# Kernel optimization log

Measured on AMD Instinct MI355X. Metric: run time of the kernel, lower is better.

Reference implementation:

```python
import jax, jax.numpy as jnp
import numpy as np

KERNEL = 11  # matches AttnBlock(kernel_size=11)
EPS = 1e-4


def _patches(x, k):
    """Extract k x k patches (stride 1, VALID), matching nn.Unfold ordering.

    x: [B, C, H, W] -> ([B, L, C*k*k], (Hp, Wp)) with L = Hp*Wp.
    """
    p = jax.lax.conv_general_dilated_patches(x, (k, k), (1, 1), 'VALID')  # [B, C*k*k, Hp, Wp]
    B, D, Hp, Wp = p.shape
    return p.reshape(B, D, Hp * Wp).transpose(0, 2, 1), (Hp, Wp)


def setup_inputs() -> dict:
    key = jax.random.key(0)
    k1, k2 = jax.random.split(key)
    im1 = jax.random.normal(k1, (4, 64, 40, 40), dtype=jnp.float32)
    im2 = jax.random.normal(k2, (4, 64, 40, 40), dtype=jnp.float32)
    return {"im1": im1, "im2": im2}


def reference(im1, im2):
    k = KERNEL
    # Dynamic per-sample filters from im1 patches, L2-normalized per patch.
    p1, _ = _patches(im1, k)                                  # [B, L, D], D = C*k*k
    norm = jnp.sqrt(jnp.sum(p1 * p1, axis=-1, keepdims=True))  # [B, L, 1]
    p1n = p1 / jnp.maximum(norm, EPS)
    # conv2d(im2, filters) with stride 1 / no padding == dot of im2 patches with filters.
    p2, (Hp, Wp) = _patches(im2, k)                           # [B, P, D], P = Hp*Wp
    scores = jnp.einsum('bld,bpd->bpl', p1n, p2)              # [B, P, L]
    out = jnp.max(scores, axis=-1)                            # max over filter (channel) dim
    B = im1.shape[0]
    return out.reshape(B, 1, Hp, Wp)
```

## Files before the change

kernel.cpp:

```cpp
#include <hip/hip_runtime.h>

#define C_    64
#define H_    40
#define W_    40
#define KS    11
#define HP    30
#define NB    4
#define NL    900
#define ND    59
#define EPSF  1e-4f
#define PCH   6
#define SCW   65
#define NINF  -3.4e38f
#define MPAD  1664
#define GSTEP 66600

typedef _Float16 f16x8 __attribute__((ext_vector_type(8)));
typedef float    f32x4 __attribute__((ext_vector_type(4)));

__global__ __launch_bounds__(1024)
void k_pack(const float* __restrict__ im2, const float* __restrict__ im1,
            _Float16* __restrict__ packed, float* __restrict__ invnorm) {
    const int b = blockIdx.x, img = blockIdx.y;
    const int tid = threadIdx.x;
    __shared__ float ssq[1600];
    __shared__ float colsum[1200];
    const float* src = (img ? im1 : im2) + b * C_ * 1600;
    _Float16* dst = packed + ((size_t)img * NB + b) * (8 * MPAD * 8);
    for (int pos = tid; pos < MPAD; pos += 1024) {
        float ss = 0.f;
        #pragma unroll
        for (int oct = 0; oct < 8; ++oct) {
            f16x8 h = {};
            if (pos < 1600) {
                #pragma unroll
                for (int j = 0; j < 8; ++j) {
                    float v = src[(oct * 8 + j) * 1600 + pos];
                    h[j] = (_Float16)v;
                    ss += v * v;
                }
            }
            *(f16x8*)&dst[(oct * MPAD + pos) * 8] = h;
        }
        if (img == 1 && pos < 1600) ssq[pos] = ss;
    }
    if (img != 1) return;
    __syncthreads();
    for (int t = tid; t < HP * W_; t += 1024) {
        int yy = t / W_, x = t - yy * W_;
        float s = 0.f;
        #pragma unroll
        for (int r = 0; r < KS; ++r) s += ssq[(yy + r) * W_ + x];
        colsum[t] = s;
    }
    __syncthreads();
    for (int t = tid; t < NL; t += 1024) {
        int ly = t / HP, lx = t - ly * HP;
        float s = 0.f;
        #pragma unroll
        for (int sx = 0; sx < KS; ++sx) s += colsum[ly * W_ + lx + sx];
        invnorm[b * NL + t] = 1.f / fmaxf(sqrtf(s), EPSF);
    }
}

__global__ __launch_bounds__(256, 3)
void k_gram(const _Float16* __restrict__ packed, _Float16* __restrict__ G) {
    const int i = blockIdx.x, j = blockIdx.y, b = blockIdx.z;
    int dd = i - j; if (dd < 0) dd = -dd;
    if (dd > 10) return;
    const int tid = threadIdx.x;
    const int w = tid >> 6, L = tid & 63, lq = L >> 4, lr = L & 15;

    __shared__ __align__(16) _Float16 smem[128 * 136];
    _Float16 (*As)[128][8] = (_Float16 (*)[128][8])smem;
    _Float16 (*Bs)[128][8] = (_Float16 (*)[128][8])(smem + 8192);

    const _Float16* pa = packed + (size_t)b * (8 * MPAD * 8);
    const _Float16* pb = packed + (size_t)(NB + b) * (8 * MPAD * 8);
    for (int t = tid; t < 1024; t += 256) {
        int oct = t >> 7, m = t & 127;
        *(f16x8*)&As[oct][m][0] = *(const f16x8*)&pa[(oct * MPAD + i * 128 + m) * 8];
        *(f16x8*)&Bs[oct][m][0] = *(const f16x8*)&pb[(oct * MPAD + j * 128 + m) * 8];
    }
    __syncthreads();

    const int mb = (w & 1) * 64, nb = (w >> 1) * 64;
    f16x8 a0[4], a1[4], b0[4], b1[4];
    #pragma unroll
    for (int q = 0; q < 4; ++q) {
        a0[q] = *(const f16x8*)&As[lq][mb + q * 16 + lr][0];
        a1[q] = *(const f16x8*)&As[4 + lq][mb + q * 16 + lr][0];
        b0[q] = *(const f16x8*)&Bs[lq][nb + q * 16 + lr][0];
        b1[q] = *(const f16x8*)&Bs[4 + lq][nb + q * 16 + lr][0];
    }
    f32x4 acc[4][4];
    #pragma unroll
    for (int mi = 0; mi < 4; ++mi)
        #pragma unroll
        for (int ni = 0; ni < 4; ++ni) {
            f32x4 c = {0.f, 0.f, 0.f, 0.f};
            c = __builtin_amdgcn_mfma_f32_16x16x32_f16(a0[mi], b0[ni], c, 0, 0, 0);
            c = __builtin_amdgcn_mfma_f32_16x16x32_f16(a1[mi], b1[ni], c, 0, 0, 0);
            acc[mi][ni] = c;
        }
    __syncthreads();
    #pragma unroll
    for (int mi = 0; mi < 4; ++mi)
        #pragma unroll
        for (int ni = 0; ni < 4; ++ni)
            #pragma unroll
            for (int rg = 0; rg < 4; ++rg)
                smem[(mb + mi * 16 + lq * 4 + rg) * 136 + nb + ni * 16 + lr] =
                    (_Float16)acc[mi][ni][rg];
    __syncthreads();
    _Float16* Gb = G + (size_t)b * (MPAD * MPAD);
    for (int t = tid; t < 2048; t += 256) {
        int row = t >> 4, seg = t & 15;
        *(f16x8*)&Gb[(size_t)(i * 128 + row) * MPAD + j * 128 + seg * 8] =
            *(const f16x8*)&smem[row * 136 + seg * 8];
    }
}

__global__ __launch_bounds__(256, 4)
void k_box(const _Float16* __restrict__ G, const float* __restrict__ invnorm,
           unsigned int* __restrict__ keys) {
    const int chunk = blockIdx.x;
    const int dy = (int)blockIdx.y - (HP - 1);
    const int b = blockIdx.z;
    const int ady = dy < 0 ? -dy : dy;
    const int rows = HP - ady;
    if (chunk * PCH >= rows) return;
    const int pyLo = dy < 0 ? -dy : 0;
    const int py0 = pyLo + chunk * PCH;
    const int P = min(PCH, rows - chunk * PCH);
    const int tid = threadIdx.x;

    __shared__ float csum[1600];
    __shared__ float scratch[HP * SCW];
    __shared__ float partials[120];
    __shared__ float sInv[HP];

    const _Float16* Gb = G + (size_t)b * (MPAD * MPAD);
    float s[8];
    const _Float16* base = nullptr;
    if (tid < 200) {
        int e = tid * 8, x2 = e / 40, x1 = e - x2 * 40;
        base = Gb + (size_t)py0 * GSTEP + x2 * MPAD + dy * 40 + x1;
        #pragma unroll
        for (int j = 0; j < 8; ++j) s[j] = 0.f;
        for (int r = 0; r < KS; ++r) {
            f16x8 q = *(const f16x8*)(base + r * GSTEP);
            #pragma unroll
            for (int j = 0; j < 8; ++j) s[j] += (float)q[j];
        }
    }

    for (int i = 0; i < P; ++i) {
        const int py = py0 + i, ly = py + dy;
        if (tid < 200) {
            if (i > 0) {
                f16x8 qa = *(const f16x8*)(base + (i + 10) * GSTEP);
                f16x8 qs = *(const f16x8*)(base + (i - 1) * GSTEP);
                #pragma unroll
                for (int j = 0; j < 8; ++j) s[j] += (float)qa[j] - (float)qs[j];
            }
            float4* c4 = (float4*)(csum + tid * 8);
            c4[0] = make_float4(s[0], s[1], s[2], s[3]);
            c4[1] = make_float4(s[4], s[5], s[6], s[7]);
        } else if (tid >= 224 && tid < 224 + HP) {
            sInv[tid - 224] = invnorm[b * NL + ly * HP + (tid - 224)];
        }
        __syncthreads();
        for (int t = tid; t < 5 * ND; t += 256) {
            int pg = t / ND, dxI = t - ND * pg;
            int dx = dxI - (HP - 1), pxb = 6 * pg;
            #pragma unroll
            for (int u = 0; u < 6; ++u) scratch[(pxb + u) * SCW + dxI] = NINF;
            int u0 = max(0, -dx - pxb), u1 = min(5, (HP - 1) - dx - pxb);
            if (u0 <= u1) {
                const float* cp = csum + dx;
                float run = 0.f;
                #pragma unroll
                for (int sr = 0; sr < KS; ++sr) run += cp[(pxb + u0 + sr) * (W_ + 1)];
                int u = u0;
                for (;;) {
                    scratch[(pxb + u) * SCW + dxI] = run * sInv[pxb + u + dx];
                    if (++u > u1) break;
                    run += cp[(pxb + u + 10) * (W_ + 1)] - cp[(pxb + u - 1) * (W_ + 1)];
                }
            }
        }
        __syncthreads();
        if (tid < 120) {
            int px = tid >> 2, q = tid & 3;
            float m = NINF;
            int d0 = q * 15, d1 = min(d0 + 15, ND);
            for (int d = d0; d < d1; ++d) m = fmaxf(m, scratch[px * SCW + d]);
            partials[tid] = m;
        }
        __syncthreads();
        if (tid < HP) {
            float m = fmaxf(fmaxf(partials[tid * 4], partials[tid * 4 + 1]),
                            fmaxf(partials[tid * 4 + 2], partials[tid * 4 + 3]));
            unsigned int ub = __float_as_uint(m);
            unsigned int k = (ub & 0x80000000u) ? ~ub : (ub | 0x80000000u);
            atomicMax(&keys[b * NL + py * HP + tid], k);
        }
        __syncthreads();
    }
}

__global__ __launch_bounds__(256)
void k_decode(const unsigned int* __restrict__ keys, float* __restrict__ out) {
    int i = blockIdx.x * 256 + threadIdx.x;
    if (i < NB * NL) {
        unsigned int k = keys[i];
        unsigned int u = (k & 0x80000000u) ? (k ^ 0x80000000u) : ~k;
        out[i] = __uint_as_float(u);
    }
}

__global__ __launch_bounds__(256)
void k_norm_fb(const float* __restrict__ im1, float* __restrict__ invnorm) {
    const int ly = blockIdx.x, b = blockIdx.y;
    const int tid = threadIdx.x;
    __shared__ float colsq[KS * W_];
    __shared__ float colsum[W_];
    const float* base = im1 + b * C_ * H_ * W_;
    for (int i = tid; i < KS * W_; i += 256) {
        int r = i / W_, x = i - r * W_;
        const float* p = base + (ly + r) * W_ + x;
        float s = 0.f;
        #pragma unroll 8
        for (int c = 0; c < C_; ++c) { float v = p[c * H_ * W_]; s += v * v; }
        colsq[i] = s;
    }
    __syncthreads();
    if (tid < W_) {
        float s = 0.f;
        #pragma unroll
        for (int r = 0; r < KS; ++r) s += colsq[r * W_ + tid];
        colsum[tid] = s;
    }
    __syncthreads();
    if (tid < HP) {
        float s = 0.f;
        #pragma unroll
        for (int sx = 0; sx < KS; ++sx) s += colsum[tid + sx];
        invnorm[b * NL + ly * HP + tid] = 1.f / fmaxf(sqrtf(s), EPSF);
    }
}

#define MAXPL 16
__global__ __launch_bounds__(256, 2)
void k_main_fb(const float* __restrict__ im1, const float* __restrict__ im2,
               const float* __restrict__ invnorm, unsigned int* __restrict__ keys) {
    const int chunk = blockIdx.x;
    const int dy = (int)blockIdx.y - (HP - 1);
    const int b = blockIdx.z;
    const int ady = dy < 0 ? -dy : dy;
    const int rows = HP - ady;
    if (chunk * PCH >= rows) return;
    const int pyLo = dy < 0 ? -dy : 0;
    const int py0 = pyLo + chunk * PCH;
    const int P = min(PCH, rows - chunk * PCH);
    const int nPl = P + KS - 1;
    const int tid = threadIdx.x;
    const int w = tid >> 6, L = tid & 63, lq = L >> 4, lr = L & 15;

    __shared__ __align__(16) _Float16 planes[MAXPL][H_ * W_];
    __shared__ __align__(16) float csum[H_ * W_];
    __shared__ __align__(16) _Float16 Astg[8][48][8];
    __shared__ __align__(16) _Float16 Bstg[8][48][8];
    __shared__ float scratch[HP * SCW];
    __shared__ float partials[120];
    __shared__ float sInv[HP];

    const float* im1b = im1 + b * C_ * H_ * W_;
    const float* im2b = im2 + b * C_ * H_ * W_;
    if (tid < 128) {
        int arr = tid >> 6, r = tid & 63;
        int oct = r >> 3, x = 40 + (r & 7);
        f16x8 z = {};
        *(f16x8*)((arr ? Bstg : Astg)[oct][x]) = z;
    }
    for (int p = 0; p < nPl; ++p) {
        const int y = py0 + p;
        for (int t = tid; t < 640; t += 256) {
            int arr = t >= 320;
            int r = arr ? t - 320 : t;
            int oct = r / 40, x = r - oct * 40;
            const float* pc = (arr ? (im1b + (y + dy) * W_) : (im2b + y * W_))
                              + oct * 8 * H_ * W_ + x;
            f16x8 h;
            #pragma unroll
            for (int j = 0; j < 8; ++j) h[j] = (_Float16)pc[j * H_ * W_];
            *(f16x8*)((arr ? Bstg : Astg)[oct][x]) = h;
        }
        __syncthreads();
        for (int t = w; t < 9; t += 4) {
            int mt = t / 3, nt = t - 3 * mt;
            f16x8 a0 = *(const f16x8*)(Astg[lq][mt * 16 + lr]);
            f16x8 b0 = *(const f16x8*)(Bstg[lq][nt * 16 + lr]);
            f16x8 a1 = *(const f16x8*)(Astg[4 + lq][mt * 16 + lr]);
            f16x8 b1 = *(const f16x8*)(Bstg[4 + lq][nt * 16 + lr]);
            f32x4 acc = {0.f, 0.f, 0.f, 0.f};
            acc = __builtin_amdgcn_mfma_f32_16x16x32_f16(a0, b0, acc, 0, 0, 0);
            acc = __builtin_amdgcn_mfma_f32_16x16x32_f16(a1, b1, acc, 0, 0, 0);
            int x1 = nt * 16 + lr;
            if (x1 < W_) {
                int x2b = mt * 16 + lq * 4;
                #pragma unroll
                for (int rg = 0; rg < 4; ++rg) {
                    int x2 = x2b + rg;
                    if (x2 < W_) planes[p][x2 * W_ + x1] = (_Float16)acc[rg];
                }
            }
        }
        __syncthreads();
    }
    for (int i = 0; i < P; ++i) {
        const int py = py0 + i, ly = py + dy;
        if (tid < 200) {
            float4* c4 = (float4*)(csum + tid * 8);
            if (i == 0) {
                float s[8] = {0.f,0.f,0.f,0.f,0.f,0.f,0.f,0.f};
                #pragma unroll
                for (int r = 0; r < KS; ++r) {
                    f16x8 q = *(const f16x8*)(planes[r] + tid * 8);
                    #pragma unroll
                    for (int j = 0; j < 8; ++j) s[j] += (float)q[j];
                }
                c4[0] = make_float4(s[0], s[1], s[2], s[3]);
                c4[1] = make_float4(s[4], s[5], s[6], s[7]);
            } else {
                f16x8 qa = *(const f16x8*)(planes[i + 10] + tid * 8);
                f16x8 qs = *(const f16x8*)(planes[i - 1] + tid * 8);
                float4 v0 = c4[0], v1 = c4[1];
                v0.x += (float)qa[0] - (float)qs[0]; v0.y += (float)qa[1] - (float)qs[1];
                v0.z += (float)qa[2] - (float)qs[2]; v0.w += (float)qa[3] - (float)qs[3];
                v1.x += (float)qa[4] - (float)qs[4]; v1.y += (float)qa[5] - (float)qs[5];
                v1.z += (float)qa[6] - (float)qs[6]; v1.w += (float)qa[7] - (float)qs[7];
                c4[0] = v0; c4[1] = v1;
            }
        } else if (tid >= 224 && tid < 224 + HP) {
            sInv[tid - 224] = invnorm[b * NL + ly * HP + (tid - 224)];
        }
        __syncthreads();
        for (int t = tid; t < 5 * ND; t += 256) {
            int pg = t / ND, dxI = t - ND * pg;
            int dx = dxI - (HP - 1), pxb = 6 * pg;
            #pragma unroll
            for (int u = 0; u < 6; ++u) scratch[(pxb + u) * SCW + dxI] = NINF;
            int u0 = max(0, -dx - pxb), u1 = min(5, (HP - 1) - dx - pxb);
            if (u0 <= u1) {
                const float* cp = csum + dx;
                float run = 0.f;
                #pragma unroll
                for (int sr = 0; sr < KS; ++sr) run += cp[(pxb + u0 + sr) * (W_ + 1)];
                int u = u0;
                for (;;) {
                    scratch[(pxb + u) * SCW + dxI] = run * sInv[pxb + u + dx];
                    if (++u > u1) break;
                    run += cp[(pxb + u + 10) * (W_ + 1)] - cp[(pxb + u - 1) * (W_ + 1)];
                }
            }
        }
        __syncthreads();
        if (tid < 120) {
            int px = tid >> 2, q = tid & 3;
            float m = NINF;
            int d0 = q * 15, d1 = min(d0 + 15, ND);
            for (int d = d0; d < d1; ++d) m = fmaxf(m, scratch[px * SCW + d]);
            partials[tid] = m;
        }
        __syncthreads();
        if (tid < HP) {
            float m = fmaxf(fmaxf(partials[tid * 4], partials[tid * 4 + 1]),
                            fmaxf(partials[tid * 4 + 2], partials[tid * 4 + 3]));
            unsigned int ub = __float_as_uint(m);
            unsigned int k = (ub & 0x80000000u) ? ~ub : (ub | 0x80000000u);
            atomicMax(&keys[b * NL + py * HP + tid], k);
        }
        __syncthreads();
    }
}

extern "C" void kernel_launch(void* const* d_in, const int* in_sizes, int n_in,
                              void* d_out, int out_size, void* d_ws, size_t ws_size,
                              hipStream_t stream) {
    const float* im1 = (const float*)d_in[0];
    const float* im2 = (const float*)d_in[1];
    unsigned int* keys = (unsigned int*)d_ws;
    float* invnorm = (float*)d_ws + NB * NL;
    const size_t packedOff = 32768;
    const size_t packedBytes = (size_t)2 * NB * 8 * MPAD * 8 * 2;
    const size_t gOff = packedOff + packedBytes;
    const size_t gBytes = (size_t)NB * MPAD * MPAD * 2;
    const size_t needed = gOff + gBytes;

    hipMemsetAsync(d_ws, 0, NB * NL * sizeof(unsigned int), stream);
    if (ws_size >= needed) {
        _Float16* packed = (_Float16*)((char*)d_ws + packedOff);
        _Float16* G = (_Float16*)((char*)d_ws + gOff);
        k_pack<<<dim3(NB, 2), 1024, 0, stream>>>(im2, im1, packed, invnorm);
        k_gram<<<dim3(13, 13, NB), 256, 0, stream>>>(packed, G);
        k_box<<<dim3(5, ND, NB), 256, 0, stream>>>(G, invnorm, keys);
    } else {
        k_norm_fb<<<dim3(HP, NB), 256, 0, stream>>>(im1, invnorm);
        k_main_fb<<<dim3(5, ND, NB), 256, 0, stream>>>(im1, im2, invnorm, keys);
    }
    k_decode<<<(NB * NL + 255) / 256, 256, 0, stream>>>(keys, (float*)d_out);
}
```

Measured before the change: 110.3 us.

## Spread packing over many blocks, fold key clearing in, prefetch box loads

The pack kernel used to run as 8 blocks of 1024 threads. It is now split across 104 small blocks and writes per-position sums of squares to a buffer. A separate small k_norm kernel turns those sums into inverse patch norms. Key zeroing moves into the pack kernel, so the memset is dropped from the fast path. In k_box, the inverse norms for every row are loaded once up front, the next row's sliding-window G loads are issued before the barrier so they overlap the scan, and the trailing barrier in each row loop is removed. The cost is one extra kernel launch in exchange for better GPU occupancy during packing and less latency in the box stage.

```diff
diff --git a/kernel.cpp b/kernel.cpp
--- a/kernel.cpp
+++ b/kernel.cpp
@@ -18,33 +18,38 @@
 typedef _Float16 f16x8 __attribute__((ext_vector_type(8)));
 typedef float    f32x4 __attribute__((ext_vector_type(4)));
 
+__global__ __launch_bounds__(128)
+void k_pack(const float* __restrict__ im2, const float* __restrict__ im1,
+            _Float16* __restrict__ packed, float* __restrict__ ssqbuf,
+            unsigned int* __restrict__ keys) {
+    const int blk = blockIdx.x, b = blockIdx.y, img = blockIdx.z;
+    const int pos = blk * 128 + threadIdx.x;
+    const float* src = (img ? im1 : im2) + b * C_ * 1600;
+    _Float16* dst = packed + ((size_t)img * NB + b) * (8 * MPAD * 8);
+    float ss = 0.f;
+    #pragma unroll
+    for (int oct = 0; oct < 8; ++oct) {
+        f16x8 h = {};
+        if (pos < 1600) {
+            #pragma unroll
+            for (int j = 0; j < 8; ++j) {
+                float v = src[(oct * 8 + j) * 1600 + pos];
+                h[j] = (_Float16)v;
+                ss += v * v;
+            }
+        }
+        *(f16x8*)&dst[(oct * MPAD + pos) * 8] = h;
+    }
+    if (img == 1 && pos < 1600) ssqbuf[b * 1600 + pos] = ss;
+    if (img == 0 && pos < NL) keys[b * NL + pos] = 0u;
+}
+
 __global__ __launch_bounds__(1024)
-void k_pack(const float* __restrict__ im2, const float* __restrict__ im1,
-            _Float16* __restrict__ packed, float* __restrict__ invnorm) {
-    const int b = blockIdx.x, img = blockIdx.y;
-    const int tid = threadIdx.x;
+void k_norm(const float* __restrict__ ssqbuf, float* __restrict__ invnorm) {
+    const int b = blockIdx.x, tid = threadIdx.x;
     __shared__ float ssq[1600];
     __shared__ float colsum[1200];
-    const float* src = (img ? im1 : im2) + b * C_ * 1600;
-    _Float16* dst = packed + ((size_t)img * NB + b) * (8 * MPAD * 8);
-    for (int pos = tid; pos < MPAD; pos += 1024) {
-        float ss = 0.f;
-        #pragma unroll
-        for (int oct = 0; oct < 8; ++oct) {
-            f16x8 h = {};
-            if (pos < 1600) {
-                #pragma unroll
-                for (int j = 0; j < 8; ++j) {
-                    float v = src[(oct * 8 + j) * 1600 + pos];
-                    h[j] = (_Float16)v;
-                    ss += v * v;
-                }
-            }
-            *(f16x8*)&dst[(oct * MPAD + pos) * 8] = h;
-        }
-        if (img == 1 && pos < 1600) ssq[pos] = ss;
-    }
-    if (img != 1) return;
+    for (int i = tid; i < 1600; i += 1024) ssq[i] = ssqbuf[b * 1600 + i];
     __syncthreads();
     for (int t = tid; t < HP * W_; t += 1024) {
         int yy = t / W_, x = t - yy * W_;
@@ -138,10 +143,16 @@
     __shared__ float csum[1600];
     __shared__ float scratch[HP * SCW];
     __shared__ float partials[120];
-    __shared__ float sInv[HP];
+    __shared__ float sInvAll[PCH][HP];
+
+    if (tid < P * HP) {
+        int i = tid / HP, lx = tid - i * HP;
+        sInvAll[i][lx] = invnorm[b * NL + (py0 + i + dy) * HP + lx];
+    }
 
     const _Float16* Gb = G + (size_t)b * (MPAD * MPAD);
     float s[8];
+    f16x8 qa, qs;
     const _Float16* base = nullptr;
     if (tid < 200) {
         int e = tid * 8, x2 = e / 40, x1 = e - x2 * 40;
@@ -156,19 +167,19 @@
     }
 
     for (int i = 0; i < P; ++i) {
-        const int py = py0 + i, ly = py + dy;
+        const int py = py0 + i;
         if (tid < 200) {
             if (i > 0) {
-                f16x8 qa = *(const f16x8*)(base + (i + 10) * GSTEP);
-                f16x8 qs = *(const f16x8*)(base + (i - 1) * GSTEP);
                 #pragma unroll
                 for (int j = 0; j < 8; ++j) s[j] += (float)qa[j] - (float)qs[j];
             }
             float4* c4 = (float4*)(csum + tid * 8);
             c4[0] = make_float4(s[0], s[1], s[2], s[3]);
             c4[1] = make_float4(s[4], s[5], s[6], s[7]);
-        } else if (tid >= 224 && tid < 224 + HP) {
-            sInv[tid - 224] = invnorm[b * NL + ly * HP + (tid - 224)];
+            if (i + 1 < P) {
+                qa = *(const f16x8*)(base + (i + 11) * GSTEP);
+                qs = *(const f16x8*)(base + i * GSTEP);
+            }
         }
         __syncthreads();
         for (int t = tid; t < 5 * ND; t += 256) {
@@ -184,7 +195,7 @@
                 for (int sr = 0; sr < KS; ++sr) run += cp[(pxb + u0 + sr) * (W_ + 1)];
                 int u = u0;
                 for (;;) {
-                    scratch[(pxb + u) * SCW + dxI] = run * sInv[pxb + u + dx];
+                    scratch[(pxb + u) * SCW + dxI] = run * sInvAll[i][pxb + u + dx];
                     if (++u > u1) break;
                     run += cp[(pxb + u + 10) * (W_ + 1)] - cp[(pxb + u - 1) * (W_ + 1)];
                 }
@@ -206,7 +217,6 @@
             unsigned int k = (ub & 0x80000000u) ? ~ub : (ub | 0x80000000u);
             atomicMax(&keys[b * NL + py * HP + tid], k);
         }
-        __syncthreads();
     }
 }
 
@@ -392,21 +402,23 @@
     const float* im1 = (const float*)d_in[0];
     const float* im2 = (const float*)d_in[1];
     unsigned int* keys = (unsigned int*)d_ws;
-    float* invnorm = (float*)d_ws + NB * NL;
-    const size_t packedOff = 32768;
+    float* invnorm = (float*)((char*)d_ws + 14400);
+    float* ssqbuf  = (float*)((char*)d_ws + 28800);
+    const size_t packedOff = 65536;
     const size_t packedBytes = (size_t)2 * NB * 8 * MPAD * 8 * 2;
     const size_t gOff = packedOff + packedBytes;
     const size_t gBytes = (size_t)NB * MPAD * MPAD * 2;
     const size_t needed = gOff + gBytes;
 
-    hipMemsetAsync(d_ws, 0, NB * NL * sizeof(unsigned int), stream);
     if (ws_size >= needed) {
         _Float16* packed = (_Float16*)((char*)d_ws + packedOff);
         _Float16* G = (_Float16*)((char*)d_ws + gOff);
-        k_pack<<<dim3(NB, 2), 1024, 0, stream>>>(im2, im1, packed, invnorm);
+        k_pack<<<dim3(13, NB, 2), 128, 0, stream>>>(im2, im1, packed, ssqbuf, keys);
+        k_norm<<<NB, 1024, 0, stream>>>(ssqbuf, invnorm);
         k_gram<<<dim3(13, 13, NB), 256, 0, stream>>>(packed, G);
         k_box<<<dim3(5, ND, NB), 256, 0, stream>>>(G, invnorm, keys);
     } else {
+        hipMemsetAsync(d_ws, 0, NB * NL * sizeof(unsigned int), stream);
         k_norm_fb<<<dim3(HP, NB), 256, 0, stream>>>(im1, invnorm);
         k_main_fb<<<dim3(5, ND, NB), 256, 0, stream>>>(im1, im2, invnorm, keys);
     }
```

Result: faster. 103.0 us (-6.6%).
